# Performance work log

Measured on AMD Instinct MI355X. Metric: run time of the kernel, lower is better.

The kernel has to match this reference:

```python
import jax, jax.numpy as jnp
import numpy as np

B, T, DIM, H, HD, K = 4, 2048, 1024, 16, 64, 4
QK = H * HD          # 1024
VD = 2 * H * HD      # 2048
EPS = 1e-5


def zrms(x, g):
    # zero-centered RMS norm with learned scale
    x = x - jnp.mean(x, axis=-1, keepdims=True)
    return x * jax.lax.rsqrt(jnp.mean(x * x, axis=-1, keepdims=True) + EPS) * g


def causal_dwconv(x, w):
    # x: [B,T,C], w: [K,1,C] (keras depthwise Conv1D kernel, groups=C)
    k = w.shape[0]
    return jax.lax.conv_general_dilated(
        x, w, window_strides=(1,), padding=[(k - 1, 0)],
        dimension_numbers=('NWC', 'WIO', 'NWC'),
        feature_group_count=x.shape[-1])


def setup_inputs() -> dict:
    key = jax.random.key(0)
    ks = jax.random.split(key, 12)
    s = lambda *sh: 1.0 / np.sqrt(sh[0])
    return {
        'x':  jax.random.normal(ks[0], (B, T, DIM), jnp.float32),
        'Wq': jax.random.normal(ks[1], (DIM, QK), jnp.float32) * s(DIM),
        'Wk': jax.random.normal(ks[2], (DIM, QK), jnp.float32) * s(DIM),
        'Wv': jax.random.normal(ks[3], (DIM, VD), jnp.float32) * s(DIM),
        'gq': jnp.ones((QK,), jnp.float32),
        'gk': jnp.ones((QK,), jnp.float32),
        'gv': jnp.ones((VD,), jnp.float32),
        'cq': jax.random.normal(ks[4], (K, 1, QK), jnp.float32) * 0.5,
        'ck': jax.random.normal(ks[5], (K, 1, QK), jnp.float32) * 0.5,
        'cv': jax.random.normal(ks[6], (K, 1, VD), jnp.float32) * 0.5,
        'Wa': jax.random.normal(ks[7], (DIM, H), jnp.float32) * s(DIM),
        'Wb': jax.random.normal(ks[8], (DIM, H), jnp.float32) * s(DIM),
        'Wo': jax.random.normal(ks[9], (VD, DIM), jnp.float32) * s(VD),
        'Wg': jax.random.normal(ks[10], (DIM, DIM), jnp.float32) * s(DIM),
    }


def reference(x, Wq, Wk, Wv, gq, gk, gv, cq, ck, cv, Wa, Wb, Wo, Wg):
    # 1) projections  2) zero-centered RMSNorm  3) causal depthwise conv (+silu)
    q = jax.nn.silu(causal_dwconv(zrms(x @ Wq, gq), cq))   # [B,T,QK]
    k = jax.nn.silu(causal_dwconv(zrms(x @ Wk, gk), ck))   # [B,T,QK]
    v = jax.nn.silu(causal_dwconv(zrms(x @ Wv, gv), cv))   # [B,T,VD]

    q = q.reshape(B, T, H, HD)
    k = k.reshape(B, T, H, HD)
    v = v.reshape(B, T, H, 2 * HD)

    # 4) per-head gating params
    alpha = jax.nn.sigmoid(x @ Wa)  # [B,T,H]
    beta = jax.nn.sigmoid(x @ Wb)   # [B,T,H]

    # 5) gated delta-rule recurrence over time (state S: [B,H,2*HD,HD])
    def step(S, inp):
        qt, kt, vt, at, bt = inp  # [B,H,HD],[B,H,HD],[B,H,2HD],[B,H],[B,H]
        a = at[..., None, None]
        upd = S + bt[..., None, None] * jnp.einsum('bhv,bhk->bhvk', vt, kt)
        S = a * upd + (1.0 - a) * S
        o = jnp.einsum('bhvk,bhk->bhv', S, qt)  # Q_t readout
        return S, o

    S0 = jnp.zeros((B, H, 2 * HD, HD), x.dtype)
    xs = (q.transpose(1, 0, 2, 3), k.transpose(1, 0, 2, 3),
          v.transpose(1, 0, 2, 3), alpha.transpose(1, 0, 2),
          beta.transpose(1, 0, 2))
    _, o = jax.lax.scan(step, S0, xs)          # o: [T,B,H,2HD]
    o = o.transpose(1, 0, 2, 3).reshape(B, T, VD)

    # 6) output projection + sigmoid output gate
    proj = o @ Wo                              # [B,T,DIM]
    return jax.nn.sigmoid(proj @ Wg) * proj
```

## Files before the change

### kernel.cpp

```cpp
#include <hip/hip_runtime.h>
#include <hip/hip_bf16.h>
#include <math.h>

#define RTOT 8192
#define TSEQ 2048

typedef __attribute__((ext_vector_type(8))) short short8;
typedef __attribute__((ext_vector_type(4))) float f32x4;
typedef unsigned short u16;
typedef unsigned int u32;

union U16x8 { uint4 v; u16 s[8]; };

__device__ __forceinline__ float sigmoidf_(float x) { return 1.f / (1.f + expf(-x)); }
__device__ __forceinline__ float bf2f(u16 v) { u32 u = ((u32)v) << 16; float f; __builtin_memcpy(&f, &u, 4); return f; }
__device__ __forceinline__ u16 f2bf(float f) {
  u32 u; __builtin_memcpy(&u, &f, 4);
  u32 r = (u + 0x7FFFu + ((u >> 16) & 1u)) >> 16;
  return (u16)r;
}
__device__ __forceinline__ void split2(float x, u16& h, u16& l) {
  u16 hh = f2bf(x);
  float hf = bf2f(hh);
  h = hh; l = f2bf(x - hf);
}

typedef const void __attribute__((address_space(1))) gvoid_t;
typedef void __attribute__((address_space(3))) lvoid_t;
__device__ __forceinline__ void gload_lds16(const void* g, void* l) {
  __builtin_amdgcn_global_load_lds((gvoid_t*)g, (lvoid_t*)l, 16, 0, 0);
}

__device__ __forceinline__ void xcd_remap(int& bx, int& by) {
  int gx = gridDim.x, nwg = gx * gridDim.y;
  int bid = blockIdx.y * gx + blockIdx.x;
  int cpx = nwg >> 3;
  int swz = (bid & 7) * cpx + (bid >> 3);
  bx = swz % gx; by = swz / gx;
}

__global__ __launch_bounds__(512) void gemm_sp_big(const u16* __restrict__ Ah, const u16* __restrict__ Al,
                                                   const u16* __restrict__ Bh, const u16* __restrict__ Bl,
                                                   float* __restrict__ Cf,
                                                   int M, int N, int K) {
  __shared__ u16 lds[2][4][256 * 32];
  int bx, by; xcd_remap(bx, by);
  const int tid = threadIdx.x;
  const int l = tid & 63, w = tid >> 6;
  const int wr = w >> 2, wc = w & 3;
  const int m0 = by * 256, n0 = bx * 256;
  const int fr = l & 15, fq = l >> 4;
  const int koff = 8 * (fq ^ (fr & 3));
  const int srow = tid >> 2;
  const int scol = ((tid & 3) ^ (srow & 3)) * 8;
  const u16* gA_h = Ah + (size_t)(m0 + srow) * K + scol;
  const u16* gA_l = Al + (size_t)(m0 + srow) * K + scol;
  const u16* gB_h = Bh + (size_t)(n0 + srow) * K + scol;
  const u16* gB_l = Bl + (size_t)(n0 + srow) * K + scol;
  const int lo = srow * 32 + (tid & 3) * 8;
  const int NT = K >> 5;

#define STAGE_QKV(buf, t)                                            \
  do {                                                               \
    const int k0_ = (t) << 5;                                        \
    gload_lds16(gA_h + k0_, &lds[buf][0][lo]);                       \
    gload_lds16(gA_h + 128 * K + k0_, &lds[buf][0][lo + 4096]);      \
    gload_lds16(gA_l + k0_, &lds[buf][1][lo]);                       \
    gload_lds16(gA_l + 128 * K + k0_, &lds[buf][1][lo + 4096]);      \
    gload_lds16(gB_h + k0_, &lds[buf][2][lo]);                       \
    gload_lds16(gB_h + 128 * K + k0_, &lds[buf][2][lo + 4096]);      \
    gload_lds16(gB_l + k0_, &lds[buf][3][lo]);                       \
    gload_lds16(gB_l + 128 * K + k0_, &lds[buf][3][lo + 4096]);      \
  } while (0)

  f32x4 acc[8][4] = {};
  STAGE_QKV(0, 0);
  STAGE_QKV(1, 1);
  asm volatile("s_waitcnt vmcnt(8)" ::: "memory");
  __builtin_amdgcn_s_barrier();

  for (int t = 0; t < NT; ++t) {
    const int cur = t & 1;
    short8 bh8[4], bl8[4];
#pragma unroll
    for (int n = 0; n < 4; ++n) {
      bh8[n] = *(const short8*)&lds[cur][2][(wc * 64 + n * 16 + fr) * 32 + koff];
      bl8[n] = *(const short8*)&lds[cur][3][(wc * 64 + n * 16 + fr) * 32 + koff];
    }
    short8 ah8[8], al8[8];
#pragma unroll
    for (int m = 0; m < 8; ++m) {
      ah8[m] = *(const short8*)&lds[cur][0][(wr * 128 + m * 16 + fr) * 32 + koff];
      al8[m] = *(const short8*)&lds[cur][1][(wr * 128 + m * 16 + fr) * 32 + koff];
    }
    __builtin_amdgcn_s_setprio(1);
#pragma unroll
    for (int m = 0; m < 8; ++m)
#pragma unroll
      for (int n = 0; n < 4; ++n) {
        acc[m][n] = __builtin_amdgcn_mfma_f32_16x16x32_bf16(ah8[m], bh8[n], acc[m][n], 0, 0, 0);
        acc[m][n] = __builtin_amdgcn_mfma_f32_16x16x32_bf16(ah8[m], bl8[n], acc[m][n], 0, 0, 0);
        acc[m][n] = __builtin_amdgcn_mfma_f32_16x16x32_bf16(al8[m], bh8[n], acc[m][n], 0, 0, 0);
      }
    __builtin_amdgcn_s_setprio(0);
    asm volatile("s_waitcnt lgkmcnt(0)" ::: "memory");
    __builtin_amdgcn_s_barrier();
    if (t + 2 < NT) {
      STAGE_QKV(cur, t + 2);
      asm volatile("s_waitcnt vmcnt(8)" ::: "memory");
    } else if (t + 1 < NT) {
      asm volatile("s_waitcnt vmcnt(0)" ::: "memory");
    }
    __builtin_amdgcn_s_barrier();
  }
#undef STAGE_QKV
#pragma unroll
  for (int m = 0; m < 8; ++m)
#pragma unroll
    for (int n = 0; n < 4; ++n)
#pragma unroll
      for (int r = 0; r < 4; ++r)
        Cf[(size_t)(m0 + wr * 128 + m * 16 + 4 * fq + r) * N + (n0 + wc * 64 + n * 16 + fr)] = acc[m][n][r];
}

template<int EPI>
__global__ __launch_bounds__(256) void gemm_sp(const u16* __restrict__ Ah, const u16* __restrict__ Al,
                                               const u16* __restrict__ Bh, const u16* __restrict__ Bl,
                                               float* __restrict__ Cf, u16* __restrict__ Ph,
                                               u16* __restrict__ Pl, const float* __restrict__ Pin,
                                               int M, int N, int K) {
  __shared__ u16 Ash[128 * 32], Asl[128 * 32];
  __shared__ u16 Bsh[128 * 32], Bsl[128 * 32];
  int bx, by; xcd_remap(bx, by);
  const int tid = threadIdx.x;
  const int l = tid & 63, w = tid >> 6;
  const int m0 = by * 128, n0 = bx * 128;
  const int wr = w >> 1, wc = w & 1;
  f32x4 acc[4][4] = {};
  const int srow = (w << 5) + (l >> 2);
  const int scol = (l & 3) << 3;
  const size_t gA = (size_t)(m0 + srow) * K + scol;
  const size_t gB = (size_t)(n0 + srow) * K + scol;
  const int lo0 = (w * 2 + 0) * 512, lo1 = (w * 2 + 1) * 512;
  const int arow = wr * 64 + (l & 15), brow = wc * 64 + (l & 15);
  const int koff = 8 * (l >> 4);
  for (int k0 = 0; k0 < K; k0 += 32) {
    gload_lds16(Ah + gA + k0, &Ash[lo0]);
    gload_lds16(Ah + gA + 16 * K + k0, &Ash[lo1]);
    gload_lds16(Al + gA + k0, &Asl[lo0]);
    gload_lds16(Al + gA + 16 * K + k0, &Asl[lo1]);
    gload_lds16(Bh + gB + k0, &Bsh[lo0]);
    gload_lds16(Bh + gB + 16 * K + k0, &Bsh[lo1]);
    gload_lds16(Bl + gB + k0, &Bsl[lo0]);
    gload_lds16(Bl + gB + 16 * K + k0, &Bsl[lo1]);
    __syncthreads();
    short8 afh[4], afl[4], bfh[4], bfl[4];
#pragma unroll
    for (int m = 0; m < 4; ++m) {
      afh[m] = *(const short8*)&Ash[(arow + m * 16) * 32 + koff];
      afl[m] = *(const short8*)&Asl[(arow + m * 16) * 32 + koff];
    }
#pragma unroll
    for (int n = 0; n < 4; ++n) {
      bfh[n] = *(const short8*)&Bsh[(brow + n * 16) * 32 + koff];
      bfl[n] = *(const short8*)&Bsl[(brow + n * 16) * 32 + koff];
    }
#pragma unroll
    for (int m = 0; m < 4; ++m)
#pragma unroll
      for (int n = 0; n < 4; ++n) {
        acc[m][n] = __builtin_amdgcn_mfma_f32_16x16x32_bf16(afh[m], bfh[n], acc[m][n], 0, 0, 0);
        acc[m][n] = __builtin_amdgcn_mfma_f32_16x16x32_bf16(afh[m], bfl[n], acc[m][n], 0, 0, 0);
        acc[m][n] = __builtin_amdgcn_mfma_f32_16x16x32_bf16(afl[m], bfh[n], acc[m][n], 0, 0, 0);
      }
    __syncthreads();
  }
  const int rbase = m0 + wr * 64 + 4 * (l >> 4);
  const int cbase = n0 + wc * 64 + (l & 15);
#pragma unroll
  for (int m = 0; m < 4; ++m)
#pragma unroll
    for (int n = 0; n < 4; ++n)
#pragma unroll
      for (int r = 0; r < 4; ++r) {
        size_t idx = (size_t)(rbase + m * 16 + r) * N + (cbase + n * 16);
        float v = acc[m][n][r];
        if (EPI == 0) {
          Cf[idx] = v;
        } else if (EPI == 1) {
          Cf[idx] = v;
          u16 h, lo; split2(v, h, lo);
          Ph[idx] = h; Pl[idx] = lo;
        } else {
          Cf[idx] = Pin[idx] * sigmoidf_(v);
        }
      }
}

__global__ __launch_bounds__(256) void transcast_sp(const float* __restrict__ W,
                                                    u16* __restrict__ Wth, u16* __restrict__ Wtl,
                                                    int K, int N) {
  __shared__ float t[32][33];
  const int n0 = blockIdx.x * 32, k0 = blockIdx.y * 32;
  const int c = threadIdx.x & 31, rq = threadIdx.x >> 5;
#pragma unroll
  for (int i = 0; i < 4; ++i) t[rq * 4 + i][c] = W[(size_t)(k0 + rq * 4 + i) * N + n0 + c];
  __syncthreads();
#pragma unroll
  for (int i = 0; i < 4; ++i) {
    float v = t[c][rq * 4 + i];
    u16 h, lo; split2(v, h, lo);
    size_t idx = (size_t)(n0 + rq * 4 + i) * K + k0 + c;
    Wth[idx] = h; Wtl[idx] = lo;
  }
}

__global__ __launch_bounds__(256) void castx_sp(const float* __restrict__ x,
                                                u16* __restrict__ xh, u16* __restrict__ xl) {
  size_t i = (size_t)blockIdx.x * 256 + threadIdx.x;
  float4 v = ((const float4*)x)[i];
  ushort4 hh, ll;
  split2(v.x, hh.x, ll.x); split2(v.y, hh.y, ll.y);
  split2(v.z, hh.z, ll.z); split2(v.w, hh.w, ll.w);
  ((ushort4*)xh)[i] = hh; ((ushort4*)xl)[i] = ll;
}

template<int C, int GSCALE>
__global__ __launch_bounds__(C / 4) void conv_fs(const float* __restrict__ zn,
                                                 const float* __restrict__ w,
                                                 const float* __restrict__ g,
                                                 const float* __restrict__ gab,
                                                 u16* __restrict__ oh,
                                                 u16* __restrict__ ol) {
  constexpr int NW = C / 256;
  __shared__ float redA[NW * 4];
  __shared__ float redB[NW * 4];
  const int tid = threadIdx.x;
  const int row = blockIdx.x;
  const int t = row & (TSEQ - 1);
  const int c = tid * 4;
  const int lane = tid & 63, wid = tid >> 6;
  float4 xv[4];
  float psum[4];
#pragma unroll
  for (int d = 0; d < 4; ++d) {
    if (t - d >= 0) xv[d] = *(const float4*)(zn + (size_t)(row - d) * 4096 + c);
    else { xv[d].x = 0.f; xv[d].y = 0.f; xv[d].z = 0.f; xv[d].w = 0.f; }
    psum[d] = xv[d].x + xv[d].y + xv[d].z + xv[d].w;
  }
#pragma unroll
  for (int d = 0; d < 4; ++d)
#pragma unroll
    for (int o = 32; o > 0; o >>= 1) psum[d] += __shfl_xor(psum[d], o, 64);
  if (lane == 0) {
    redA[wid * 4 + 0] = psum[0]; redA[wid * 4 + 1] = psum[1];
    redA[wid * 4 + 2] = psum[2]; redA[wid * 4 + 3] = psum[3];
  }
  __syncthreads();
  float mean[4];
#pragma unroll
  for (int d = 0; d < 4; ++d) {
    float s = 0.f;
#pragma unroll
    for (int j = 0; j < NW; ++j) s += redA[j * 4 + d];
    mean[d] = s * (1.f / C);
  }
  float psq[4];
#pragma unroll
  for (int d = 0; d < 4; ++d) {
    float a = xv[d].x - mean[d], b = xv[d].y - mean[d];
    float e = xv[d].z - mean[d], f = xv[d].w - mean[d];
    psq[d] = a * a + b * b + e * e + f * f;
  }
#pragma unroll
  for (int d = 0; d < 4; ++d)
#pragma unroll
    for (int o = 32; o > 0; o >>= 1) psq[d] += __shfl_xor(psq[d], o, 64);
  if (lane == 0) {
    redB[wid * 4 + 0] = psq[0]; redB[wid * 4 + 1] = psq[1];
    redB[wid * 4 + 2] = psq[2]; redB[wid * 4 + 3] = psq[3];
  }
  __syncthreads();
  float rstd[4];
#pragma unroll
  for (int d = 0; d < 4; ++d) {
    float s = 0.f;
#pragma unroll
    for (int j = 0; j < NW; ++j) s += redB[j * 4 + d];
    rstd[d] = rsqrtf(s * (1.f / C) + 1e-5f);
  }
  float4 g4 = *(const float4*)(g + c);
  float4 acc; acc.x = 0.f; acc.y = 0.f; acc.z = 0.f; acc.w = 0.f;
#pragma unroll
  for (int d = 0; d < 4; ++d) {
    if (t - d >= 0) {
      float4 wv = *(const float4*)(w + (size_t)(3 - d) * C + c);
      acc.x = fmaf((xv[d].x - mean[d]) * rstd[d] * g4.x, wv.x, acc.x);
      acc.y = fmaf((xv[d].y - mean[d]) * rstd[d] * g4.y, wv.y, acc.y);
      acc.z = fmaf((xv[d].z - mean[d]) * rstd[d] * g4.z, wv.z, acc.z);
      acc.w = fmaf((xv[d].w - mean[d]) * rstd[d] * g4.w, wv.w, acc.w);
    }
  }
  float a0 = acc.x * sigmoidf_(acc.x);
  float a1 = acc.y * sigmoidf_(acc.y);
  float a2 = acc.z * sigmoidf_(acc.z);
  float a3 = acc.w * sigmoidf_(acc.w);
  if (GSCALE) {
    float gv = gab[(size_t)row * 16 + (c >> 7)];
    a0 *= gv; a1 *= gv; a2 *= gv; a3 *= gv;
  }
  ushort4 hh, ll;
  split2(a0, hh.x, ll.x); split2(a1, hh.y, ll.y);
  split2(a2, hh.z, ll.z); split2(a3, hh.w, ll.w);
  *(ushort4*)(oh + (size_t)row * C + c) = hh;
  *(ushort4*)(ol + (size_t)row * C + c) = ll;
}

__global__ __launch_bounds__(256) void gab_kernel(const float* __restrict__ x,
                                                  const float* __restrict__ Wa,
                                                  const float* __restrict__ Wb,
                                                  float* __restrict__ gout) {
  __shared__ float xs[1024];
  __shared__ float partial[256];
  const int tid = threadIdx.x;
  const size_t row = blockIdx.x;
  *(float4*)(&xs[tid*4]) = *(const float4*)(x + row*1024 + tid*4);
  __syncthreads();
  const int h = tid & 31;
  const int seg = tid >> 5;
  const float* W = (h < 16) ? Wa : Wb;
  const int col = h & 15;
  float s = 0.f;
  const int k0 = seg * 128;
  for (int k = 0; k < 128; ++k) s = fmaf(xs[k0 + k], W[(size_t)(k0 + k) * 16 + col], s);
  partial[tid] = s;
  __syncthreads();
  if (tid < 32) {
    float t2 = 0.f;
#pragma unroll
    for (int j = 0; j < 8; ++j) t2 += partial[j*32 + tid];
    partial[tid] = t2;
  }
  __syncthreads();
  if (tid < 16)
    gout[row*16 + tid] = sigmoidf_(partial[tid]) * sigmoidf_(partial[tid + 16]);
}

__global__ __launch_bounds__(256) void scan_kernel(const u16* __restrict__ kh,
                                                   const u16* __restrict__ kl,
                                                   const u16* __restrict__ vgh,
                                                   const u16* __restrict__ vgl,
                                                   u16* __restrict__ Sph,
                                                   u16* __restrict__ Spl) {
  __shared__ float Ks[64][36];
  __shared__ float Vs[64][36];
  const int tid = threadIdx.x;
  const int bid = blockIdx.x;
  const int kq = bid & 1, vq = (bid >> 1) & 3, h = (bid >> 3) & 15, b = bid >> 7;
  const size_t rb = (size_t)b * TSEQ;
  const int vd_t = tid >> 3, kd0 = (tid & 7) * 4;
  float S[4] = {};
  const int sr = tid >> 2;
  const int cc0 = (tid & 3) * 8;
  for (int c = 0; c < 32; ++c) {
    {
      size_t koffg = (rb + (size_t)c * 64 + sr) * 1024 + h * 64 + kq * 32 + cc0;
      U16x8 a0, b0;
      a0.v = *(const uint4*)(kh + koffg);
      b0.v = *(const uint4*)(kl + koffg);
#pragma unroll
      for (int j = 0; j < 8; ++j) Ks[sr][cc0 + j] = bf2f(a0.s[j]) + bf2f(b0.s[j]);
      size_t voffg = (rb + (size_t)c * 64 + sr) * 2048 + h * 128 + vq * 32 + cc0;
      U16x8 va, vb;
      va.v = *(const uint4*)(vgh + voffg);
      vb.v = *(const uint4*)(vgl + voffg);
#pragma unroll
      for (int j = 0; j < 8; ++j) Vs[sr][cc0 + j] = bf2f(va.s[j]) + bf2f(vb.s[j]);
    }
    {
      size_t spc = (((size_t)(b * 16 + h) * 32) + c) * 8192
                 + (size_t)(vq * 32 + vd_t) * 64 + kq * 32 + kd0;
      ushort4 h0, l0;
      split2(S[0], h0.x, l0.x); split2(S[1], h0.y, l0.y);
      split2(S[2], h0.z, l0.z); split2(S[3], h0.w, l0.w);
      *(ushort4*)(Sph + spc) = h0;
      *(ushort4*)(Spl + spc) = l0;
    }
    __syncthreads();
    for (int s = 0; s < 64; ++s) {
      float vv = Vs[s][vd_t];
      float kv[4];
      *(float4*)kv = *(const float4*)&Ks[s][kd0];
#pragma unroll
      for (int j = 0; j < 4; ++j) S[j] = fmaf(vv, kv[j], S[j]);
    }
    __syncthreads();
  }
}

__global__ __launch_bounds__(256) void pass2_sp(const u16* __restrict__ qh,
                                                const u16* __restrict__ ql,
                                                const u16* __restrict__ kh,
                                                const u16* __restrict__ vgh,
                                                const u16* __restrict__ Sph,
                                                const u16* __restrict__ Spl,
                                                u16* __restrict__ oh,
                                                u16* __restrict__ ol) {
  __shared__ u16 Qsh[64 * 72];
  __shared__ u16 Qsl[64 * 72];
  __shared__ u16 Ksm[64 * 72];
  __shared__ u16 Am[64 * 72];
  __shared__ u16 Vth[128 * 72];
  const int tid = threadIdx.x;
  const int l = tid & 63, w = tid >> 6;
  const int bid = blockIdx.x;
  const int c = bid & 31, h = (bid >> 5) & 15, b = bid >> 9;
  const size_t rb = (size_t)b * TSEQ + c * 64;
  const int fr = l & 15, fq = l >> 4;
  {
    int r = tid >> 2, c0 = (tid & 3) * 16;
    size_t off = (rb + r) * 1024 + h * 64 + c0;
    *(uint4*)&Qsh[r * 72 + c0]     = *(const uint4*)(qh + off);
    *(uint4*)&Qsh[r * 72 + c0 + 8] = *(const uint4*)(qh + off + 8);
    *(uint4*)&Qsl[r * 72 + c0]     = *(const uint4*)(ql + off);
    *(uint4*)&Qsl[r * 72 + c0 + 8] = *(const uint4*)(ql + off + 8);
    *(uint4*)&Ksm[r * 72 + c0]     = *(const uint4*)(kh + off);
    *(uint4*)&Ksm[r * 72 + c0 + 8] = *(const uint4*)(kh + off + 8);
  }
  {
    int s = tid >> 2, vd0 = (tid & 3) * 32;
    size_t off = (rb + s) * 2048 + h * 128 + vd0;
#pragma unroll
    for (int m4 = 0; m4 < 4; ++m4) {
      U16x8 r_; r_.v = *(const uint4*)(vgh + off + m4 * 8);
#pragma unroll
      for (int j = 0; j < 8; ++j) Vth[(vd0 + m4 * 8 + j) * 72 + s] = r_.s[j];
    }
  }
  __syncthreads();
  short8 aqh[2], aql[2];
#pragma unroll
  for (int kk = 0; kk < 2; ++kk) {
    aqh[kk] = *(const short8*)&Qsh[(w * 16 + fr) * 72 + kk * 32 + 8 * fq];
    aql[kk] = *(const short8*)&Qsl[(w * 16 + fr) * 72 + kk * 32 + 8 * fq];
  }
  f32x4 accA[4] = {};
#pragma unroll
  for (int n = 0; n < 4; ++n)
#pragma unroll
    for (int kk = 0; kk < 2; ++kk) {
      short8 bk = *(const short8*)&Ksm[(n * 16 + fr) * 72 + kk * 32 + 8 * fq];
      accA[n] = __builtin_amdgcn_mfma_f32_16x16x32_bf16(aqh[kk], bk, accA[n], 0, 0, 0);
    }
#pragma unroll
  for (int n = 0; n < 4; ++n)
#pragma unroll
    for (int rr = 0; rr < 4; ++rr) {
      int tt = w * 16 + 4 * fq + rr;
      int s = n * 16 + fr;
      Am[tt * 72 + s] = f2bf((s <= tt) ? accA[n][rr] : 0.f);
    }
  __syncthreads();
  f32x4 acc[8] = {};
#pragma unroll
  for (int kk = 0; kk < 2; ++kk) {
    short8 aa = *(const short8*)&Am[(w * 16 + fr) * 72 + kk * 32 + 8 * fq];
#pragma unroll
    for (int n = 0; n < 8; ++n) {
      short8 bv = *(const short8*)&Vth[(n * 16 + fr) * 72 + kk * 32 + 8 * fq];
      acc[n] = __builtin_amdgcn_mfma_f32_16x16x32_bf16(aa, bv, acc[n], 0, 0, 0);
    }
  }
  const size_t spb = (((size_t)(b * 16 + h) * 32) + c) * 8192;
#pragma unroll
  for (int n = 0; n < 8; ++n)
#pragma unroll
    for (int kk = 0; kk < 2; ++kk) {
      size_t soff = spb + (size_t)(n * 16 + fr) * 64 + kk * 32 + 8 * fq;
      short8 bh_ = *(const short8*)(Sph + soff);
      short8 bl_ = *(const short8*)(Spl + soff);
      acc[n] = __builtin_amdgcn_mfma_f32_16x16x32_bf16(aqh[kk], bh_, acc[n], 0, 0, 0);
      acc[n] = __builtin_amdgcn_mfma_f32_16x16x32_bf16(aqh[kk], bl_, acc[n], 0, 0, 0);
      acc[n] = __builtin_amdgcn_mfma_f32_16x16x32_bf16(aql[kk], bh_, acc[n], 0, 0, 0);
    }
#pragma unroll
  for (int n = 0; n < 8; ++n)
#pragma unroll
    for (int rr = 0; rr < 4; ++rr) {
      int tt = w * 16 + 4 * fq + rr;
      int vd = n * 16 + fr;
      u16 hh, ll;
      split2(acc[n][rr], hh, ll);
      size_t off = (rb + tt) * 2048 + h * 128 + vd;
      oh[off] = hh; ol[off] = ll;
    }
}

extern "C" void kernel_launch(void* const* d_in, const int* in_sizes, int n_in,
                              void* d_out, int out_size, void* d_ws, size_t ws_size,
                              hipStream_t stream) {
  (void)in_sizes; (void)n_in; (void)out_size; (void)ws_size;
  const float* x  = (const float*)d_in[0];
  const float* Wq = (const float*)d_in[1];
  const float* Wk = (const float*)d_in[2];
  const float* Wv = (const float*)d_in[3];
  const float* gq = (const float*)d_in[4];
  const float* gk = (const float*)d_in[5];
  const float* gv = (const float*)d_in[6];
  const float* cq = (const float*)d_in[7];
  const float* ck = (const float*)d_in[8];
  const float* cv = (const float*)d_in[9];
  const float* Wa = (const float*)d_in[10];
  const float* Wb = (const float*)d_in[11];
  const float* Wo = (const float*)d_in[12];
  const float* Wg = (const float*)d_in[13];
  float* out = (float*)d_out;
  char* ws = (char*)d_ws;

  const size_t MiB = 1024 * 1024;
  u16* Wqkv_h = (u16*)(ws + 0 * MiB);
  u16* Wqkv_l = (u16*)(ws + 8 * MiB);
  u16* Wo_h   = (u16*)(ws + 16 * MiB);
  u16* Wo_l   = (u16*)(ws + 20 * MiB);
  u16* Wg_h   = (u16*)(ws + 24 * MiB);
  u16* Wg_l   = (u16*)(ws + 26 * MiB);
  float* gbuf = (float*)(ws + 28 * MiB);
  u16* x_h    = (u16*)(ws + 32 * MiB);
  u16* x_l    = (u16*)(ws + 48 * MiB);
  float* qkv  = (float*)(ws + 64 * MiB);
  u16* q_h = (u16*)(ws + 192 * MiB);
  u16* q_l = (u16*)(ws + 208 * MiB);
  u16* k_h = (u16*)(ws + 224 * MiB);
  u16* k_l = (u16*)(ws + 240 * MiB);
  u16* vg_h = (u16*)(ws + 32 * MiB);
  u16* vg_l = (u16*)d_out;
  u16* Sp_h = (u16*)(ws + 96 * MiB);
  u16* Sp_l = (u16*)(ws + 128 * MiB);
  u16* o_h  = (u16*)(ws + 64 * MiB);
  u16* o_l  = (u16*)d_out;
  float* proj = (float*)(ws + 96 * MiB);
  u16* p_h  = (u16*)(ws + 128 * MiB);
  u16* p_l  = (u16*)(ws + 144 * MiB);

  dim3 blk(256);
  castx_sp<<<dim3(8192), blk, 0, stream>>>(x, x_h, x_l);
  transcast_sp<<<dim3(32, 32), blk, 0, stream>>>(Wq, Wqkv_h, Wqkv_l, 1024, 1024);
  transcast_sp<<<dim3(32, 32), blk, 0, stream>>>(Wk, Wqkv_h + 1024 * 1024, Wqkv_l + 1024 * 1024, 1024, 1024);
  transcast_sp<<<dim3(64, 32), blk, 0, stream>>>(Wv, Wqkv_h + 2048 * 1024, Wqkv_l + 2048 * 1024, 1024, 2048);
  transcast_sp<<<dim3(32, 64), blk, 0, stream>>>(Wo, Wo_h, Wo_l, 2048, 1024);
  transcast_sp<<<dim3(32, 32), blk, 0, stream>>>(Wg, Wg_h, Wg_l, 1024, 1024);
  gab_kernel<<<dim3(8192), blk, 0, stream>>>(x, Wa, Wb, gbuf);
  gemm_sp_big<<<dim3(16, 32), dim3(512), 0, stream>>>(x_h, x_l, Wqkv_h, Wqkv_l, qkv, 8192, 4096, 1024);
  conv_fs<1024, 0><<<dim3(8192), dim3(256), 0, stream>>>(qkv, cq, gq, nullptr, q_h, q_l);
  conv_fs<1024, 0><<<dim3(8192), dim3(256), 0, stream>>>(qkv + 1024, ck, gk, nullptr, k_h, k_l);
  conv_fs<2048, 1><<<dim3(8192), dim3(512), 0, stream>>>(qkv + 2048, cv, gv, gbuf, vg_h, vg_l);
  scan_kernel<<<dim3(512), blk, 0, stream>>>(k_h, k_l, vg_h, vg_l, Sp_h, Sp_l);
  pass2_sp<<<dim3(2048), blk, 0, stream>>>(q_h, q_l, k_h, vg_h, Sp_h, Sp_l, o_h, o_l);
  gemm_sp<1><<<dim3(8, 64), blk, 0, stream>>>(o_h, o_l, Wo_h, Wo_l, proj, p_h, p_l, nullptr, 8192, 1024, 2048);
  gemm_sp<2><<<dim3(8, 64), blk, 0, stream>>>(p_h, p_l, Wg_h, Wg_l, out, nullptr, nullptr, proj, 8192, 1024, 1024);
}
```

Before: 676.0 us.

## Split QKV GEMM K-step into four phases interleaving prefetch with MFMA

Restructures the main loop of the 256x256 split-bf16 QKV GEMM. Each K-step now runs in four phases that load two A fragments from LDS, issue part of the next tile's global-to-LDS prefetch, and run the MFMAs, with barriers between phases. It replaces the depth-2 prefetch (two tiles in flight) with a depth-1 ping-pong and lowers register pressure by holding only two A fragments at a time. The cost is many more barriers per K-step and a shallower prefetch that may expose memory latency.

```diff
diff --git a/kernel.cpp b/kernel.cpp
--- a/kernel.cpp
+++ b/kernel.cpp
@@ -60,60 +60,95 @@
   const int lo = srow * 32 + (tid & 3) * 8;
   const int NT = K >> 5;
 
-#define STAGE_QKV(buf, t)                                            \
-  do {                                                               \
-    const int k0_ = (t) << 5;                                        \
-    gload_lds16(gA_h + k0_, &lds[buf][0][lo]);                       \
-    gload_lds16(gA_h + 128 * K + k0_, &lds[buf][0][lo + 4096]);      \
-    gload_lds16(gA_l + k0_, &lds[buf][1][lo]);                       \
-    gload_lds16(gA_l + 128 * K + k0_, &lds[buf][1][lo + 4096]);      \
-    gload_lds16(gB_h + k0_, &lds[buf][2][lo]);                       \
-    gload_lds16(gB_h + 128 * K + k0_, &lds[buf][2][lo + 4096]);      \
-    gload_lds16(gB_l + k0_, &lds[buf][3][lo]);                       \
-    gload_lds16(gB_l + 128 * K + k0_, &lds[buf][3][lo + 4096]);      \
+#define STG(buf, mat, src, t)                                 \
+  do {                                                        \
+    const int k0_ = (t) << 5;                                 \
+    gload_lds16(src + k0_, &lds[buf][mat][lo]);               \
+    gload_lds16(src + 128 * K + k0_, &lds[buf][mat][lo + 4096]); \
   } while (0)
 
+#define MFMA_PAIR(mi, a_h, a_l)                                                        \
+  do {                                                                                 \
+    _Pragma("unroll")                                                                  \
+    for (int n = 0; n < 4; ++n) {                                                      \
+      acc[mi][n] = __builtin_amdgcn_mfma_f32_16x16x32_bf16(a_h, bh8[n], acc[mi][n], 0, 0, 0); \
+      acc[mi][n] = __builtin_amdgcn_mfma_f32_16x16x32_bf16(a_h, bl8[n], acc[mi][n], 0, 0, 0); \
+      acc[mi][n] = __builtin_amdgcn_mfma_f32_16x16x32_bf16(a_l, bh8[n], acc[mi][n], 0, 0, 0); \
+    }                                                                                  \
+  } while (0)
+
   f32x4 acc[8][4] = {};
-  STAGE_QKV(0, 0);
-  STAGE_QKV(1, 1);
-  asm volatile("s_waitcnt vmcnt(8)" ::: "memory");
+  STG(0, 0, gA_h, 0); STG(0, 1, gA_l, 0); STG(0, 2, gB_h, 0); STG(0, 3, gB_l, 0);
+  asm volatile("s_waitcnt vmcnt(0)" ::: "memory");
   __builtin_amdgcn_s_barrier();
 
   for (int t = 0; t < NT; ++t) {
-    const int cur = t & 1;
+    const int c = t & 1, o = c ^ 1;
+    const bool pf = (t + 1 < NT);
     short8 bh8[4], bl8[4];
-#pragma unroll
-    for (int n = 0; n < 4; ++n) {
-      bh8[n] = *(const short8*)&lds[cur][2][(wc * 64 + n * 16 + fr) * 32 + koff];
-      bl8[n] = *(const short8*)&lds[cur][3][(wc * 64 + n * 16 + fr) * 32 + koff];
-    }
-    short8 ah8[8], al8[8];
-#pragma unroll
-    for (int m = 0; m < 8; ++m) {
-      ah8[m] = *(const short8*)&lds[cur][0][(wr * 128 + m * 16 + fr) * 32 + koff];
-      al8[m] = *(const short8*)&lds[cur][1][(wr * 128 + m * 16 + fr) * 32 + koff];
-    }
-    __builtin_amdgcn_s_setprio(1);
-#pragma unroll
-    for (int m = 0; m < 8; ++m)
+    {
 #pragma unroll
       for (int n = 0; n < 4; ++n) {
-        acc[m][n] = __builtin_amdgcn_mfma_f32_16x16x32_bf16(ah8[m], bh8[n], acc[m][n], 0, 0, 0);
-        acc[m][n] = __builtin_amdgcn_mfma_f32_16x16x32_bf16(ah8[m], bl8[n], acc[m][n], 0, 0, 0);
-        acc[m][n] = __builtin_amdgcn_mfma_f32_16x16x32_bf16(al8[m], bh8[n], acc[m][n], 0, 0, 0);
+        bh8[n] = *(const short8*)&lds[c][2][(wc * 64 + n * 16 + fr) * 32 + koff];
+        bl8[n] = *(const short8*)&lds[c][3][(wc * 64 + n * 16 + fr) * 32 + koff];
       }
-    __builtin_amdgcn_s_setprio(0);
-    asm volatile("s_waitcnt lgkmcnt(0)" ::: "memory");
-    __builtin_amdgcn_s_barrier();
-    if (t + 2 < NT) {
-      STAGE_QKV(cur, t + 2);
-      asm volatile("s_waitcnt vmcnt(8)" ::: "memory");
-    } else if (t + 1 < NT) {
-      asm volatile("s_waitcnt vmcnt(0)" ::: "memory");
-    }
-    __builtin_amdgcn_s_barrier();
-  }
-#undef STAGE_QKV
+      short8 a0h = *(const short8*)&lds[c][0][(wr * 128 + 0 * 16 + fr) * 32 + koff];
+      short8 a1h = *(const short8*)&lds[c][0][(wr * 128 + 1 * 16 + fr) * 32 + koff];
+      short8 a0l = *(const short8*)&lds[c][1][(wr * 128 + 0 * 16 + fr) * 32 + koff];
+      short8 a1l = *(const short8*)&lds[c][1][(wr * 128 + 1 * 16 + fr) * 32 + koff];
+      if (pf) { STG(o, 2, gB_h, t + 1); STG(o, 3, gB_l, t + 1); }
+      __builtin_amdgcn_s_barrier();
+      asm volatile("s_waitcnt lgkmcnt(0)" ::: "memory");
+      __builtin_amdgcn_s_setprio(1);
+      MFMA_PAIR(0, a0h, a0l);
+      MFMA_PAIR(1, a1h, a1l);
+      __builtin_amdgcn_s_setprio(0);
+      __builtin_amdgcn_s_barrier();
+    }
+    {
+      short8 a0h = *(const short8*)&lds[c][0][(wr * 128 + 2 * 16 + fr) * 32 + koff];
+      short8 a1h = *(const short8*)&lds[c][0][(wr * 128 + 3 * 16 + fr) * 32 + koff];
+      short8 a0l = *(const short8*)&lds[c][1][(wr * 128 + 2 * 16 + fr) * 32 + koff];
+      short8 a1l = *(const short8*)&lds[c][1][(wr * 128 + 3 * 16 + fr) * 32 + koff];
+      if (pf) { STG(o, 0, gA_h, t + 1); STG(o, 1, gA_l, t + 1); }
+      __builtin_amdgcn_s_barrier();
+      asm volatile("s_waitcnt lgkmcnt(0)" ::: "memory");
+      __builtin_amdgcn_s_setprio(1);
+      MFMA_PAIR(2, a0h, a0l);
+      MFMA_PAIR(3, a1h, a1l);
+      __builtin_amdgcn_s_setprio(0);
+      __builtin_amdgcn_s_barrier();
+    }
+    {
+      short8 a0h = *(const short8*)&lds[c][0][(wr * 128 + 4 * 16 + fr) * 32 + koff];
+      short8 a1h = *(const short8*)&lds[c][0][(wr * 128 + 5 * 16 + fr) * 32 + koff];
+      short8 a0l = *(const short8*)&lds[c][1][(wr * 128 + 4 * 16 + fr) * 32 + koff];
+      short8 a1l = *(const short8*)&lds[c][1][(wr * 128 + 5 * 16 + fr) * 32 + koff];
+      __builtin_amdgcn_s_barrier();
+      asm volatile("s_waitcnt lgkmcnt(0)" ::: "memory");
+      __builtin_amdgcn_s_setprio(1);
+      MFMA_PAIR(4, a0h, a0l);
+      MFMA_PAIR(5, a1h, a1l);
+      __builtin_amdgcn_s_setprio(0);
+      __builtin_amdgcn_s_barrier();
+    }
+    {
+      short8 a0h = *(const short8*)&lds[c][0][(wr * 128 + 6 * 16 + fr) * 32 + koff];
+      short8 a1h = *(const short8*)&lds[c][0][(wr * 128 + 7 * 16 + fr) * 32 + koff];
+      short8 a0l = *(const short8*)&lds[c][1][(wr * 128 + 6 * 16 + fr) * 32 + koff];
+      short8 a1l = *(const short8*)&lds[c][1][(wr * 128 + 7 * 16 + fr) * 32 + koff];
+      __builtin_amdgcn_s_barrier();
+      asm volatile("s_waitcnt lgkmcnt(0)" ::: "memory");
+      __builtin_amdgcn_s_setprio(1);
+      MFMA_PAIR(6, a0h, a0l);
+      MFMA_PAIR(7, a1h, a1l);
+      __builtin_amdgcn_s_setprio(0);
+      if (pf) asm volatile("s_waitcnt vmcnt(0)" ::: "memory");
+      __builtin_amdgcn_s_barrier();
+    }
+  }
+#undef STG
+#undef MFMA_PAIR
 #pragma unroll
   for (int m = 0; m < 8; ++m)
 #pragma unroll
```

After: 671.9 us. No clear change (-0.6%).

## Split QKV GEMM k-step into three phases with per-matrix interleaved prefetch

Applied to the files above, without the earlier changes.

Restructures the split-bf16 QKV GEMM main loop from a whole-tile double buffer with a prefetch distance of two into three phases per k-step (hi*hi, hi*lo, lo*hi). Each phase issues the global-to-LDS prefetch of the next tile's matrix and waits only for the current tile's operands it needs. The goal is to overlap load latency with MFMA work at finer granularity and reduce register pressure from holding all fragments at once. In exchange it adds more barriers per iteration, and the prefetch distance drops to one tile, which may expose memory latency.

```diff
diff --git a/kernel.cpp b/kernel.cpp
--- a/kernel.cpp
+++ b/kernel.cpp
@@ -60,60 +60,78 @@
   const int lo = srow * 32 + (tid & 3) * 8;
   const int NT = K >> 5;
 
-#define STAGE_QKV(buf, t)                                            \
-  do {                                                               \
-    const int k0_ = (t) << 5;                                        \
-    gload_lds16(gA_h + k0_, &lds[buf][0][lo]);                       \
-    gload_lds16(gA_h + 128 * K + k0_, &lds[buf][0][lo + 4096]);      \
-    gload_lds16(gA_l + k0_, &lds[buf][1][lo]);                       \
-    gload_lds16(gA_l + 128 * K + k0_, &lds[buf][1][lo + 4096]);      \
-    gload_lds16(gB_h + k0_, &lds[buf][2][lo]);                       \
-    gload_lds16(gB_h + 128 * K + k0_, &lds[buf][2][lo + 4096]);      \
-    gload_lds16(gB_l + k0_, &lds[buf][3][lo]);                       \
-    gload_lds16(gB_l + 128 * K + k0_, &lds[buf][3][lo + 4096]);      \
+#define STG(buf, mat, src, t)                                 \
+  do {                                                        \
+    const int k0_ = (t) << 5;                                 \
+    gload_lds16(src + k0_, &lds[buf][mat][lo]);               \
+    gload_lds16(src + 128 * K + k0_, &lds[buf][mat][lo + 4096]); \
   } while (0)
 
   f32x4 acc[8][4] = {};
-  STAGE_QKV(0, 0);
-  STAGE_QKV(1, 1);
-  asm volatile("s_waitcnt vmcnt(8)" ::: "memory");
+  STG(0, 0, gA_h, 0); STG(0, 2, gB_h, 0); STG(0, 3, gB_l, 0); STG(0, 1, gA_l, 0);
+  asm volatile("s_waitcnt vmcnt(0)" ::: "memory");
   __builtin_amdgcn_s_barrier();
 
   for (int t = 0; t < NT; ++t) {
-    const int cur = t & 1;
-    short8 bh8[4], bl8[4];
-#pragma unroll
-    for (int n = 0; n < 4; ++n) {
-      bh8[n] = *(const short8*)&lds[cur][2][(wc * 64 + n * 16 + fr) * 32 + koff];
-      bl8[n] = *(const short8*)&lds[cur][3][(wc * 64 + n * 16 + fr) * 32 + koff];
-    }
-    short8 ah8[8], al8[8];
-#pragma unroll
-    for (int m = 0; m < 8; ++m) {
-      ah8[m] = *(const short8*)&lds[cur][0][(wr * 128 + m * 16 + fr) * 32 + koff];
-      al8[m] = *(const short8*)&lds[cur][1][(wr * 128 + m * 16 + fr) * 32 + koff];
-    }
-    __builtin_amdgcn_s_setprio(1);
-#pragma unroll
-    for (int m = 0; m < 8; ++m)
-#pragma unroll
-      for (int n = 0; n < 4; ++n) {
-        acc[m][n] = __builtin_amdgcn_mfma_f32_16x16x32_bf16(ah8[m], bh8[n], acc[m][n], 0, 0, 0);
-        acc[m][n] = __builtin_amdgcn_mfma_f32_16x16x32_bf16(ah8[m], bl8[n], acc[m][n], 0, 0, 0);
-        acc[m][n] = __builtin_amdgcn_mfma_f32_16x16x32_bf16(al8[m], bh8[n], acc[m][n], 0, 0, 0);
-      }
-    __builtin_amdgcn_s_setprio(0);
-    asm volatile("s_waitcnt lgkmcnt(0)" ::: "memory");
-    __builtin_amdgcn_s_barrier();
-    if (t + 2 < NT) {
-      STAGE_QKV(cur, t + 2);
-      asm volatile("s_waitcnt vmcnt(8)" ::: "memory");
-    } else if (t + 1 < NT) {
-      asm volatile("s_waitcnt vmcnt(0)" ::: "memory");
-    }
-    __builtin_amdgcn_s_barrier();
-  }
-#undef STAGE_QKV
+    const int c = t & 1, o = c ^ 1;
+    const bool pf = (t + 1 < NT);
+    short8 ah8[8], al8[8], bh8[4], bl8[4];
+    {
+      if (pf) { STG(o, 0, gA_h, t + 1); STG(o, 2, gB_h, t + 1); }
+      if (pf) asm volatile("s_waitcnt vmcnt(8)" ::: "memory");
+      else    asm volatile("s_waitcnt vmcnt(4)" ::: "memory");
+      __builtin_amdgcn_s_barrier();
+#pragma unroll
+      for (int m = 0; m < 8; ++m)
+        ah8[m] = *(const short8*)&lds[c][0][(wr * 128 + m * 16 + fr) * 32 + koff];
+#pragma unroll
+      for (int n = 0; n < 4; ++n)
+        bh8[n] = *(const short8*)&lds[c][2][(wc * 64 + n * 16 + fr) * 32 + koff];
+      asm volatile("s_waitcnt lgkmcnt(0)" ::: "memory");
+      __builtin_amdgcn_s_setprio(1);
+#pragma unroll
+      for (int m = 0; m < 8; ++m)
+#pragma unroll
+        for (int n = 0; n < 4; ++n)
+          acc[m][n] = __builtin_amdgcn_mfma_f32_16x16x32_bf16(ah8[m], bh8[n], acc[m][n], 0, 0, 0);
+      __builtin_amdgcn_s_setprio(0);
+    }
+    {
+      if (pf) STG(o, 3, gB_l, t + 1);
+      if (pf) asm volatile("s_waitcnt vmcnt(8)" ::: "memory");
+      else    asm volatile("s_waitcnt vmcnt(2)" ::: "memory");
+      __builtin_amdgcn_s_barrier();
+#pragma unroll
+      for (int n = 0; n < 4; ++n)
+        bl8[n] = *(const short8*)&lds[c][3][(wc * 64 + n * 16 + fr) * 32 + koff];
+      asm volatile("s_waitcnt lgkmcnt(0)" ::: "memory");
+      __builtin_amdgcn_s_setprio(1);
+#pragma unroll
+      for (int m = 0; m < 8; ++m)
+#pragma unroll
+        for (int n = 0; n < 4; ++n)
+          acc[m][n] = __builtin_amdgcn_mfma_f32_16x16x32_bf16(ah8[m], bl8[n], acc[m][n], 0, 0, 0);
+      __builtin_amdgcn_s_setprio(0);
+    }
+    {
+      if (pf) STG(o, 1, gA_l, t + 1);
+      if (pf) asm volatile("s_waitcnt vmcnt(8)" ::: "memory");
+      else    asm volatile("s_waitcnt vmcnt(0)" ::: "memory");
+      __builtin_amdgcn_s_barrier();
+#pragma unroll
+      for (int m = 0; m < 8; ++m)
+        al8[m] = *(const short8*)&lds[c][1][(wr * 128 + m * 16 + fr) * 32 + koff];
+      asm volatile("s_waitcnt lgkmcnt(0)" ::: "memory");
+      __builtin_amdgcn_s_setprio(1);
+#pragma unroll
+      for (int m = 0; m < 8; ++m)
+#pragma unroll
+        for (int n = 0; n < 4; ++n)
+          acc[m][n] = __builtin_amdgcn_mfma_f32_16x16x32_bf16(al8[m], bh8[n], acc[m][n], 0, 0, 0);
+      __builtin_amdgcn_s_setprio(0);
+    }
+  }
+#undef STG
 #pragma unroll
   for (int m = 0; m < 8; ++m)
 #pragma unroll
```

New measurement: 795.0 us. 1.18x slower.
